# Performance work log

Measured on AMD Instinct MI355X. Metric: run time of the kernel, lower is better.

## Reference

```python
import jax, jax.numpy as jnp
import numpy as np

# ---- static config (matches init_kwargs) ----
BATCH = 8; SEQ_LEN = 1024; ENC_IN = 7; PRED_LEN = 96
D_MODEL = 512; N_HEADS = 8; D_HEAD = D_MODEL // N_HEADS
D_FF = 2048; E_LAYERS = 2; FACTOR = 5
PATCH = 16; STRIDE = 8; PAD = 8
N_PATCH = (SEQ_LEN + PAD - PATCH) // STRIDE + 1  # 128
NF = D_MODEL * N_PATCH


def _sin_pe(n, d):
    # sinusoidal positional embedding (Informer/TSLib PositionalEmbedding)
    pos = np.arange(n, dtype=np.float32)[:, None]
    div = np.exp(np.arange(0, d, 2, dtype=np.float32) * (-np.log(10000.0) / d))
    pe = np.zeros((n, d), dtype=np.float32)
    pe[:, 0::2] = np.sin(pos * div)
    pe[:, 1::2] = np.cos(pos * div)
    return jnp.asarray(pe)


def _ln(x, g, b, eps=1e-5):
    m = x.mean(-1, keepdims=True)
    v = x.var(-1, keepdims=True)
    return (x - m) / jnp.sqrt(v + eps) * g + b


def _prob_attention(q, k, v, layer_idx):
    # Informer ProbAttention, mask_flag=False. q,k,v: [B,H,L,Dh]
    B, H, L, Dh = q.shape
    u = min(int(FACTOR * np.ceil(np.log(L))), L)  # sample_k == n_top here (L_Q == L_K)
    skey = jax.random.fold_in(jax.random.key(42), layer_idx)
    samp = jax.random.randint(skey, (L, u), 0, L)          # random keys per query
    k_s = k[:, :, samp, :]                                  # [B,H,L,u,Dh]
    qk_s = jnp.einsum('bhld,bhlsd->bhls', q, k_s)           # sampled scores
    M = qk_s.max(-1) - qk_s.mean(-1)                        # sparsity measure [B,H,L]
    top = jax.lax.top_k(M, u)[1]                            # active query idx [B,H,u]
    q_r = jnp.take_along_axis(q, top[..., None], axis=2)    # [B,H,u,Dh]
    scores = jnp.einsum('bhud,bhld->bhul', q_r, k) / jnp.sqrt(jnp.asarray(Dh, q.dtype))
    attn = jax.nn.softmax(scores, axis=-1)
    upd = jnp.einsum('bhul,bhld->bhud', attn, v)            # [B,H,u,Dh]
    ctx = jnp.broadcast_to(v.mean(axis=2, keepdims=True), (B, H, L, Dh))
    bi = jnp.arange(B)[:, None, None]
    hi = jnp.arange(H)[None, :, None]
    ctx = ctx.at[bi, hi, top].set(upd)                      # scatter updated queries
    return ctx


def reference(x_enc, x_mark_enc, x_dec, x_mark_dec, patch_W,
              Wq, bq, Wk, bk, Wv, bv, Wo, bo,
              c1W, c1b, c2W, c2b, ln1g, ln1b, ln2g, ln2b,
              encg, encb, headW, headb):
    B, L, C = x_enc.shape
    # Normalize('Stat'): per-series mean/std over time
    mean = x_enc.mean(axis=1, keepdims=True)
    std = jnp.sqrt(x_enc.var(axis=1, keepdims=True) + 1e-5)
    xn = (x_enc - mean) / std
    # PatchEmbedding: [B,C,L] -> replication-pad -> unfold -> linear + pos emb
    xc = jnp.pad(xn.transpose(0, 2, 1), ((0, 0), (0, 0), (0, PAD)), mode='edge')
    idx = np.arange(N_PATCH)[:, None] * STRIDE + np.arange(PATCH)
    tok = xc[:, :, idx].reshape(B * C, N_PATCH, PATCH) @ patch_W.T  # [BC,N,dm]
    tok = tok + _sin_pe(N_PATCH, D_MODEL)
    # Transformer encoder with ProbAttention
    for l in range(E_LAYERS):
        Beff, N, _ = tok.shape
        q = (tok @ Wq[l].T + bq[l]).reshape(Beff, N, N_HEADS, D_HEAD).transpose(0, 2, 1, 3)
        k = (tok @ Wk[l].T + bk[l]).reshape(Beff, N, N_HEADS, D_HEAD).transpose(0, 2, 1, 3)
        v = (tok @ Wv[l].T + bv[l]).reshape(Beff, N, N_HEADS, D_HEAD).transpose(0, 2, 1, 3)
        ctx = _prob_attention(q, k, v, l).transpose(0, 2, 1, 3).reshape(Beff, N, D_MODEL)
        x1 = _ln(tok + ctx @ Wo[l].T + bo[l], ln1g[l], ln1b[l])
        y = jax.nn.gelu(x1 @ c1W[l].T + c1b[l], approximate=False)  # conv1d k=1 == linear
        y = y @ c2W[l].T + c2b[l]
        tok = _ln(x1 + y, ln2g[l], ln2b[l])
    tok = _ln(tok, encg, encb)
    # FlattenHead: [B,C,N,dm] -> [B,C,dm,N] -> flatten -> linear -> [B,pred,C]
    feat = tok.reshape(B, C, N_PATCH, D_MODEL).transpose(0, 1, 3, 2).reshape(B, C, NF)
    dec = (feat @ headW.T + headb).transpose(0, 2, 1)
    return dec * std + mean  # de-normalize


def setup_inputs():
    key = jax.random.key(0)
    ks = iter(jax.random.split(key, 40))
    def rn(shape, s=0.02):
        return jax.random.normal(next(ks), shape, jnp.float32) * s
    return {
        'x_enc': jax.random.normal(next(ks), (BATCH, SEQ_LEN, ENC_IN), jnp.float32),
        'x_mark_enc': jax.random.normal(next(ks), (BATCH, SEQ_LEN, 4), jnp.float32),
        'x_dec': jax.random.normal(next(ks), (BATCH, 144, ENC_IN), jnp.float32),
        'x_mark_dec': jax.random.normal(next(ks), (BATCH, 144, 4), jnp.float32),
        'patch_W': rn((D_MODEL, PATCH)),
        'Wq': rn((E_LAYERS, D_MODEL, D_MODEL)), 'bq': jnp.zeros((E_LAYERS, D_MODEL)),
        'Wk': rn((E_LAYERS, D_MODEL, D_MODEL)), 'bk': jnp.zeros((E_LAYERS, D_MODEL)),
        'Wv': rn((E_LAYERS, D_MODEL, D_MODEL)), 'bv': jnp.zeros((E_LAYERS, D_MODEL)),
        'Wo': rn((E_LAYERS, D_MODEL, D_MODEL)), 'bo': jnp.zeros((E_LAYERS, D_MODEL)),
        'c1W': rn((E_LAYERS, D_FF, D_MODEL)), 'c1b': jnp.zeros((E_LAYERS, D_FF)),
        'c2W': rn((E_LAYERS, D_MODEL, D_FF)), 'c2b': jnp.zeros((E_LAYERS, D_MODEL)),
        'ln1g': jnp.ones((E_LAYERS, D_MODEL)), 'ln1b': jnp.zeros((E_LAYERS, D_MODEL)),
        'ln2g': jnp.ones((E_LAYERS, D_MODEL)), 'ln2b': jnp.zeros((E_LAYERS, D_MODEL)),
        'encg': jnp.ones((D_MODEL,)), 'encb': jnp.zeros((D_MODEL,)),
        'headW': rn((PRED_LEN, NF)), 'headb': jnp.zeros((PRED_LEN,)),
    }
```

## Files before the change

kernel.cpp:

```cpp
#include <hip/hip_runtime.h>
#include <math.h>
#include <stdint.h>

#define SEQ   1024
#define CIN   7
#define NB    8
#define BC    56
#define NP    128
#define DM    512
#define NH    8
#define DH    64
#define DFF   2048
#define U     25
#define NTOK  (BC*NP)
#define PE_COEF (-9.210340371976184f / 512.0f)
#define HKB   256
#define HNB   256

typedef __attribute__((ext_vector_type(8))) short short8;
typedef __attribute__((ext_vector_type(4))) float f32x4;

__device__ __forceinline__ short f2bf(float x) {
    union { float f; uint32_t u; } v; v.f = x;
    uint32_t r = v.u + 0x7FFFu + ((v.u >> 16) & 1u);
    return (short)(r >> 16);
}
__device__ __forceinline__ float bf2f(short x) {
    union { uint32_t u; float f; } v; v.u = ((uint32_t)(uint16_t)x) << 16;
    return v.f;
}

__device__ __forceinline__ void gl_lds16(const void* g, void* s) {
    __builtin_amdgcn_global_load_lds((const __attribute__((address_space(1))) void*)g,
                                     (__attribute__((address_space(3))) void*)s, 16, 0, 0);
}

__global__ void stats_kernel(const float* __restrict__ x, float* __restrict__ mean,
                             float* __restrict__ stdv) {
    int bc = blockIdx.x; int b = bc / CIN, c = bc % CIN;
    const float* base = x + (size_t)b * SEQ * CIN + c;
    float s = 0.f, ss = 0.f;
    for (int i = threadIdx.x; i < SEQ; i += 256) {
        float v = base[(size_t)i * CIN];
        s += v; ss += v * v;
    }
    __shared__ float rs[256], rss[256];
    rs[threadIdx.x] = s; rss[threadIdx.x] = ss; __syncthreads();
    for (int o = 128; o > 0; o >>= 1) {
        if (threadIdx.x < o) { rs[threadIdx.x] += rs[threadIdx.x + o]; rss[threadIdx.x] += rss[threadIdx.x + o]; }
        __syncthreads();
    }
    if (threadIdx.x == 0) {
        float m = rs[0] / SEQ;
        float v = rss[0] / SEQ - m * m;
        mean[bc] = m;
        stdv[bc] = sqrtf(v + 1e-5f);
    }
}

__device__ __forceinline__ void tf_round(uint32_t& x0, uint32_t& x1, uint32_t r) {
    x0 += x1; x1 = (x1 << r) | (x1 >> (32u - r)); x1 ^= x0;
}
__device__ void threefry2x32(uint32_t k0, uint32_t k1, uint32_t x0, uint32_t x1,
                             uint32_t& o0, uint32_t& o1) {
    uint32_t ks[3] = { k0, k1, k0 ^ k1 ^ 0x1BD11BDAu };
    x0 += ks[0]; x1 += ks[1];
    const uint32_t rotA[4] = {13u, 15u, 26u, 6u}, rotB[4] = {17u, 29u, 16u, 24u};
    #pragma unroll
    for (int i = 0; i < 5; i++) {
        const uint32_t* rr = (i & 1) ? rotB : rotA;
        tf_round(x0, x1, rr[0]); tf_round(x0, x1, rr[1]);
        tf_round(x0, x1, rr[2]); tf_round(x0, x1, rr[3]);
        x0 += ks[(i + 1) % 3];
        x1 += ks[(i + 2) % 3] + (uint32_t)(i + 1);
    }
    o0 = x0; o1 = x1;
}

__global__ void prep_weights(const float* __restrict__ Wq, const float* __restrict__ Wk,
                             const float* __restrict__ Wv, const float* __restrict__ bq,
                             const float* __restrict__ bk, const float* __restrict__ bv,
                             const float* __restrict__ Wo, const float* __restrict__ c1W,
                             const float* __restrict__ c2W,
                             short* __restrict__ wqkv, float* __restrict__ bqkv,
                             short* __restrict__ wo_b, short* __restrict__ c1w_b,
                             short* __restrict__ c2w_b, int* __restrict__ samp) {
    int blk = blockIdx.x, tid = threadIdx.x;
    if (blk < 1536) {
        int idx = blk * 256 + tid;
        int k4 = idx & 127;
        int n  = (idx >> 7) % 1536;
        int l  = idx / (1536 * 128);
        int sel3 = n >> 9;
        int nn = n & 511;
        const float* src = sel3 == 0 ? Wq : sel3 == 1 ? Wk : Wv;
        float4 v = *(const float4*)(src + ((size_t)l * DM + nn) * DM + k4 * 4);
        short4 o; o.x = f2bf(v.x); o.y = f2bf(v.y); o.z = f2bf(v.z); o.w = f2bf(v.w);
        *(short4*)(wqkv + ((size_t)l * 1536 + n) * DM + k4 * 4) = o;
        if (k4 == 0) {
            const float* bsrc = sel3 == 0 ? bq : sel3 == 1 ? bk : bv;
            bqkv[l * 1536 + n] = bsrc[l * DM + nn];
        }
    } else if (blk < 6144) {
        const float* in; short* out; int i;
        if (blk < 2048)      { in = Wo;  out = wo_b;  i = (blk - 1536) * 256 + tid; }
        else if (blk < 4096) { in = c1W; out = c1w_b; i = (blk - 2048) * 256 + tid; }
        else                 { in = c2W; out = c2w_b; i = (blk - 4096) * 256 + tid; }
        float4 v = ((const float4*)in)[i];
        short4 o; o.x = f2bf(v.x); o.y = f2bf(v.y); o.z = f2bf(v.z); o.w = f2bf(v.w);
        ((short4*)out)[i] = o;
    } else {
        int l = blk - 6144;
        uint32_t s0, s1; threefry2x32(0u, 42u, 0u, (uint32_t)l, s0, s1);
        uint32_t a0, a1, b0, b1;
        threefry2x32(s0, s1, 0u, 2u, a0, a1);
        threefry2x32(s0, s1, 1u, 3u, b0, b1);
        uint32_t k20 = a1, k21 = b1;
        for (int i = tid; i < 1600; i += 256) {
            uint32_t o0, o1;
            threefry2x32(k20, k21, (uint32_t)i, (uint32_t)(1600 + i), o0, o1);
            samp[l * 3200 + i]        = (int)(o0 & 127u);
            samp[l * 3200 + 1600 + i] = (int)(o1 & 127u);
        }
    }
}

__global__ void patch_embed(const float* __restrict__ x, const float* __restrict__ pw,
                            const float* __restrict__ mean, const float* __restrict__ stdv,
                            short* __restrict__ tokb) {
    int p = blockIdx.x, bc = blockIdx.y;
    int b = bc / CIN, c = bc % CIN;
    __shared__ float xs[16];
    if (threadIdx.x < 16) {
        int i = p * 8 + threadIdx.x;
        if (i > SEQ - 1) i = SEQ - 1;
        xs[threadIdx.x] = (x[(size_t)b * SEQ * CIN + (size_t)i * CIN + c] - mean[bc]) / stdv[bc];
    }
    __syncthreads();
    for (int d = threadIdx.x; d < DM; d += blockDim.x) {
        float acc = 0.f;
        const float* wr = pw + d * 16;
        #pragma unroll
        for (int t = 0; t < 16; t++) acc += xs[t] * wr[t];
        int k2 = d & ~1;
        float ang = (float)p * __expf((float)k2 * PE_COEF);
        acc += (d & 1) ? __cosf(ang) : __sinf(ang);
        tokb[((size_t)bc * NP + p) * DM + d] = f2bf(acc);
    }
}

template<int ACT>
__global__ __launch_bounds__(256) void gemm_mfma(const short* __restrict__ A,
                                                 const short* __restrict__ W,
                                                 const float* __restrict__ bias,
                                                 short* __restrict__ Cb,
                                                 int M, int N, int K) {
    __shared__ short LDSU[2][16384];
    int tid = threadIdx.x;
    int w = tid >> 6, lane = tid & 63;
    int row0 = blockIdx.x * 128, col0 = blockIdx.y * 128;
    int wrow = (w >> 1) * 64, wcol = (w & 1) * 64;
    int nt = K >> 6;
    f32x4 acc[4][4] = {};

    auto stage = [&](int b, int kt) {
        #pragma unroll
        for (int i = 0; i < 4; i++) {
            int L = i * 4096 + w * 1024 + lane * 16;
            int row = L >> 7;
            int cb  = L & 127;
            int scb = cb ^ ((row & 7) << 4);
            gl_lds16(A + (size_t)(row0 + row) * K + kt + (scb >> 1),
                     (char*)&LDSU[b][0] + i * 4096 + w * 1024);
            gl_lds16(W + (size_t)(col0 + row) * K + kt + (scb >> 1),
                     (char*)&LDSU[b][8192] + i * 4096 + w * 1024);
        }
    };

    stage(0, 0);
    __syncthreads();
    int cur = 0;
    for (int t = 0; t < nt; t++) {
        if (t + 1 < nt) stage(cur ^ 1, (t + 1) * 64);
        const char* Ab = (const char*)&LDSU[cur][0];
        const char* Bb = (const char*)&LDSU[cur][8192];
        #pragma unroll
        for (int ks = 0; ks < 2; ks++) {
            int cb = ks * 64 + ((lane >> 4) << 4);
            short8 af[4], bfr[4];
            #pragma unroll
            for (int m = 0; m < 4; m++) {
                int r = wrow + m * 16 + (lane & 15);
                af[m] = *(const short8*)(Ab + r * 128 + (cb ^ ((r & 7) << 4)));
            }
            #pragma unroll
            for (int n = 0; n < 4; n++) {
                int r = wcol + n * 16 + (lane & 15);
                bfr[n] = *(const short8*)(Bb + r * 128 + (cb ^ ((r & 7) << 4)));
            }
            #pragma unroll
            for (int m = 0; m < 4; m++)
                #pragma unroll
                for (int n = 0; n < 4; n++)
                    acc[m][n] = __builtin_amdgcn_mfma_f32_16x16x32_bf16(af[m], bfr[n], acc[m][n], 0, 0, 0);
        }
        __syncthreads();
        cur ^= 1;
    }

    #pragma unroll
    for (int m = 0; m < 4; m++) {
        int rbase = row0 + wrow + m * 16 + ((lane >> 4) << 2);
        #pragma unroll
        for (int n = 0; n < 4; n++) {
            int col = col0 + wcol + n * 16 + (lane & 15);
            float bval = bias[col];
            #pragma unroll
            for (int j = 0; j < 4; j++) {
                float v = acc[m][n][j] + bval;
                if (ACT == 1) {
                    float u = 0.7978845608f * (v + 0.044715f * v * v * v);
                    float e = exp2f(2.8853900817779268f * u);
                    v = v - v / (e + 1.0f);
                }
                Cb[(size_t)(rbase + j) * N + col] = f2bf(v);
            }
        }
    }
}

__global__ __launch_bounds__(256) void gemm_mfma64(const short* __restrict__ A,
                                                   const short* __restrict__ W,
                                                   const float* __restrict__ bias,
                                                   const short* __restrict__ residb,
                                                   short* __restrict__ Cb,
                                                   int M, int N, int K) {
    __shared__ short LDSU[2][12288];
    int tid = threadIdx.x;
    int w = tid >> 6, lane = tid & 63;
    int row0 = blockIdx.x * 64, col0 = blockIdx.y * 128;
    int nt = K >> 6;
    f32x4 acc[4][2] = {};

    auto stage = [&](int b, int kt) {
        #pragma unroll
        for (int i = 0; i < 2; i++) {
            int L = (i * 4 + w) * 1024 + lane * 16;
            int row = L >> 7, cb = L & 127;
            int scb = cb ^ ((row & 7) << 4);
            gl_lds16(A + (size_t)(row0 + row) * K + kt + (scb >> 1),
                     (char*)&LDSU[b][0] + (i * 4 + w) * 1024);
        }
        #pragma unroll
        for (int i = 0; i < 4; i++) {
            int L = (i * 4 + w) * 1024 + lane * 16;
            int row = L >> 7, cb = L & 127;
            int scb = cb ^ ((row & 7) << 4);
            gl_lds16(W + (size_t)(col0 + row) * K + kt + (scb >> 1),
                     (char*)&LDSU[b][4096] + (i * 4 + w) * 1024);
        }
    };

    stage(0, 0);
    __syncthreads();
    int cur = 0;
    for (int t = 0; t < nt; t++) {
        if (t + 1 < nt) stage(cur ^ 1, (t + 1) * 64);
        const char* Ab = (const char*)&LDSU[cur][0];
        const char* Bb = (const char*)&LDSU[cur][4096];
        #pragma unroll
        for (int ks = 0; ks < 2; ks++) {
            int cb = ks * 64 + ((lane >> 4) << 4);
            short8 af[4], bfr[2];
            #pragma unroll
            for (int m = 0; m < 4; m++) {
                int r = m * 16 + (lane & 15);
                af[m] = *(const short8*)(Ab + r * 128 + (cb ^ ((r & 7) << 4)));
            }
            #pragma unroll
            for (int n = 0; n < 2; n++) {
                int r = w * 32 + n * 16 + (lane & 15);
                bfr[n] = *(const short8*)(Bb + r * 128 + (cb ^ ((r & 7) << 4)));
            }
            #pragma unroll
            for (int m = 0; m < 4; m++)
                #pragma unroll
                for (int n = 0; n < 2; n++)
                    acc[m][n] = __builtin_amdgcn_mfma_f32_16x16x32_bf16(af[m], bfr[n], acc[m][n], 0, 0, 0);
        }
        __syncthreads();
        cur ^= 1;
    }

    #pragma unroll
    for (int m = 0; m < 4; m++) {
        int rbase = row0 + m * 16 + ((lane >> 4) << 2);
        #pragma unroll
        for (int n = 0; n < 2; n++) {
            int col = col0 + w * 32 + n * 16 + (lane & 15);
            float bval = bias[col];
            #pragma unroll
            for (int j = 0; j < 4; j++) {
                float v = acc[m][n][j] + bval + bf2f(residb[(size_t)(rbase + j) * N + col]);
                Cb[(size_t)(rbase + j) * N + col] = f2bf(v);
            }
        }
    }
}

__global__ __launch_bounds__(256, 2) void attn_fused(const short* __restrict__ qkvb,
                                                     const int* __restrict__ samp,
                                                     short* __restrict__ ctxb) {
    __shared__ float Sbuf[64 * 130];
    __shared__ short Vt[64 * 128];
    __shared__ short Kls[128 * 64];
    __shared__ float Mv[128];
    __shared__ int   topl[32];
    __shared__ float vmean[64];
    __shared__ float vpart[256];

    float* Stop = Sbuf;
    short* Pb   = (short*)(Sbuf + 32 * 130);

    int bh = blockIdx.x, bc = bh >> 3, h = bh & 7;
    int tid = threadIdx.x, w = tid >> 6, lane = tid & 63;
    const short* base = qkvb + (size_t)bc * NP * 1536 + h * DH;
    short* cbase = ctxb + (size_t)bc * NP * DM + h * DH;

    for (int e = tid; e < 1024; e += 256) {
        int row = e >> 3, c8 = e & 7;
        short8 kv = *(const short8*)(base + (size_t)row * 1536 + 512 + c8 * 8);
        *(short8*)((char*)Kls + row * 128 + ((c8 * 16) ^ ((row & 7) << 4))) = kv;
        short8 vv = *(const short8*)(base + (size_t)row * 1536 + 1024 + c8 * 8);
        #pragma unroll
        for (int j = 0; j < 8; j++) {
            int d = c8 * 8 + j;
            *(short*)((char*)Vt + d * 256 + ((2 * row) ^ ((d & 7) << 4))) = vv[j];
        }
    }
    __syncthreads();
    {
        int d = tid & 63, part = tid >> 6;
        float s = 0.f;
        #pragma unroll
        for (int i4 = 0; i4 < 4; i4++) {
            short8 v = *(const short8*)((char*)Vt + d * 256 + ((part * 64 + i4 * 16) ^ ((d & 7) << 4)));
            #pragma unroll
            for (int j = 0; j < 8; j++) s += bf2f(v[j]);
        }
        vpart[part * 64 + d] = s;
    }

    for (int half = 0; half < 2; half++) {
        int ar = half * 64 + 16 * w + (lane & 15);
        const short* qp = base + (size_t)ar * 1536;
        short8 a0 = *(const short8*)(qp + (lane >> 4) * 8);
        short8 a1 = *(const short8*)(qp + 32 + (lane >> 4) * 8);
        #pragma unroll 2
        for (int ct = 0; ct < 8; ct++) {
            int br = ct * 16 + (lane & 15);
            int cb0 = (lane >> 4) * 16;
            short8 b0 = *(const short8*)((char*)Kls + br * 128 + (cb0 ^ ((br & 7) << 4)));
            short8 b1 = *(const short8*)((char*)Kls + br * 128 + ((cb0 + 64) ^ ((br & 7) << 4)));
            f32x4 acc = {};
            acc = __builtin_amdgcn_mfma_f32_16x16x32_bf16(a0, b0, acc, 0, 0, 0);
            acc = __builtin_amdgcn_mfma_f32_16x16x32_bf16(a1, b1, acc, 0, 0, 0);
            int r0 = 16 * w + ((lane >> 4) << 2);
            int c = ct * 16 + (lane & 15);
            #pragma unroll
            for (int j = 0; j < 4; j++) Sbuf[(r0 + j) * 130 + c] = acc[j] * 0.125f;
        }
        __syncthreads();
        if (tid < 64) {
            int r = half * 64 + tid;
            const int* sp = samp + r * U;
            const float* Srow = &Sbuf[tid * 130];
            float mx = -1e30f, sm = 0.f;
            #pragma unroll
            for (int s = 0; s < U; s++) { float v = Srow[sp[s]]; mx = fmaxf(mx, v); sm += v; }
            Mv[r] = mx - sm * (1.0f / U);
        } else if (half == 0 && tid < 128) {
            int d = tid - 64;
            vmean[d] = (vpart[d] + vpart[64 + d] + vpart[128 + d] + vpart[192 + d]) * (1.0f / 128.0f);
        }
        __syncthreads();
    }

    if (w == 0) {
        float v0 = Mv[lane], v1 = Mv[lane + 64];
        for (int it = 0; it < U; it++) {
            float bv; int bi;
            if (v1 > v0) { bv = v1; bi = lane + 64; } else { bv = v0; bi = lane; }
            #pragma unroll
            for (int o = 32; o > 0; o >>= 1) {
                float ov = __shfl_xor(bv, o);
                int   oi = __shfl_xor(bi, o);
                if (ov > bv || (ov == bv && oi < bi)) { bv = ov; bi = oi; }
            }
            if (lane == 0) topl[it] = bi;
            if (bi == lane) v0 = -1e30f;
            if (bi == lane + 64) v1 = -1e30f;
        }
    } else {
        for (int e = tid - 64; e < 128 * 16; e += 192) {
            int n = e >> 4, c4 = e & 15;
            short4 o;
            o.x = f2bf(vmean[c4 * 4 + 0]); o.y = f2bf(vmean[c4 * 4 + 1]);
            o.z = f2bf(vmean[c4 * 4 + 2]); o.w = f2bf(vmean[c4 * 4 + 3]);
            *(short4*)(cbase + (size_t)n * DM + c4 * 4) = o;
        }
    }
    __syncthreads();

    {
        int rt = w & 1, cth = w >> 1;
        int u = rt * 16 + (lane & 15);
        int qrow = topl[u < U ? u : U - 1];
        const short* qp = base + (size_t)qrow * 1536;
        short8 a0 = *(const short8*)(qp + (lane >> 4) * 8);
        short8 a1 = *(const short8*)(qp + 32 + (lane >> 4) * 8);
        #pragma unroll
        for (int cti = 0; cti < 4; cti++) {
            int ct = cth * 4 + cti;
            int br = ct * 16 + (lane & 15);
            int cb0 = (lane >> 4) * 16;
            short8 b0 = *(const short8*)((char*)Kls + br * 128 + (cb0 ^ ((br & 7) << 4)));
            short8 b1 = *(const short8*)((char*)Kls + br * 128 + ((cb0 + 64) ^ ((br & 7) << 4)));
            f32x4 acc = {};
            acc = __builtin_amdgcn_mfma_f32_16x16x32_bf16(a0, b0, acc, 0, 0, 0);
            acc = __builtin_amdgcn_mfma_f32_16x16x32_bf16(a1, b1, acc, 0, 0, 0);
            int r0 = rt * 16 + ((lane >> 4) << 2);
            int c = ct * 16 + (lane & 15);
            #pragma unroll
            for (int j = 0; j < 4; j++) Stop[(r0 + j) * 130 + c] = acc[j] * 0.125f;
        }
    }
    __syncthreads();

    for (int e = tid; e < 7 * 128; e += 256)
        Pb[(25 + (e >> 7)) * 128 + (e & 127)] = 0;
    for (int it = w; it < U; it += 4) {
        float s0 = Stop[it * 130 + lane], s1 = Stop[it * 130 + 64 + lane];
        float mx = fmaxf(s0, s1);
        #pragma unroll
        for (int o = 32; o > 0; o >>= 1) mx = fmaxf(mx, __shfl_xor(mx, o));
        float e0 = expf(s0 - mx), e1 = expf(s1 - mx);
        float sum = e0 + e1;
        #pragma unroll
        for (int o = 32; o > 0; o >>= 1) sum += __shfl_xor(sum, o);
        float inv = 1.0f / sum;
        int sw = (it & 7) << 4;
        *(short*)((char*)Pb + it * 256 + ((2 * lane) ^ sw))        = f2bf(e0 * inv);
        *(short*)((char*)Pb + it * 256 + ((2 * (64 + lane)) ^ sw)) = f2bf(e1 * inv);
    }
    __syncthreads();

    #pragma unroll
    for (int t = w * 2; t < w * 2 + 2; t++) {
        int rt = t >> 2, ct = t & 3;
        int pr = rt * 16 + (lane & 15);
        int vr = ct * 16 + (lane & 15);
        f32x4 acc = {};
        #pragma unroll
        for (int ks = 0; ks < 4; ks++) {
            int off = ks * 64 + (lane >> 4) * 16;
            short8 a = *(const short8*)((char*)Pb + pr * 256 + (off ^ ((pr & 7) << 4)));
            short8 b = *(const short8*)((char*)Vt + vr * 256 + (off ^ ((vr & 7) << 4)));
            acc = __builtin_amdgcn_mfma_f32_16x16x32_bf16(a, b, acc, 0, 0, 0);
        }
        int u0 = rt * 16 + ((lane >> 4) << 2), d = ct * 16 + (lane & 15);
        #pragma unroll
        for (int j = 0; j < 4; j++) {
            int u = u0 + j;
            if (u < U) cbase[(size_t)topl[u] * DM + d] = f2bf(acc[j]);
        }
    }
}

__global__ __launch_bounds__(256) void residual_ln(const short* __restrict__ a,
                                                   const float* __restrict__ g,
                                                   const float* __restrict__ beta,
                                                   short* __restrict__ outb) {
    int row = blockIdx.x;
    int tid = threadIdx.x;
    uint32_t va = ((const uint32_t*)(a + (size_t)row * DM))[tid];
    float x0 = bf2f((short)(va & 0xffff));
    float x1 = bf2f((short)(va >> 16));
    __shared__ float rs[256], rss[256];
    rs[tid] = x0 + x1; rss[tid] = x0 * x0 + x1 * x1; __syncthreads();
    for (int o = 128; o > 0; o >>= 1) {
        if (tid < o) { rs[tid] += rs[tid + o]; rss[tid] += rss[tid + o]; }
        __syncthreads();
    }
    float m = rs[0] / DM;
    float var = rss[0] / DM - m * m;
    float r = rsqrtf(var + 1e-5f);
    float2 gg = ((const float2*)g)[tid];
    float2 bb = ((const float2*)beta)[tid];
    float y0 = (x0 - m) * r * gg.x + bb.x;
    float y1 = (x1 - m) * r * gg.y + bb.y;
    uint32_t vo = (uint32_t)(uint16_t)f2bf(y0) | ((uint32_t)(uint16_t)f2bf(y1) << 16);
    ((uint32_t*)(outb + (size_t)row * DM))[tid] = vo;
}

__global__ void transpose_tok(const short* __restrict__ tokb, short* __restrict__ featb) {
    __shared__ short t[32][34];
    int bc = blockIdx.z, dt = blockIdx.y, pt = blockIdx.x;
    int tx = threadIdx.x, ty = threadIdx.y;
    #pragma unroll
    for (int i = 0; i < 4; i++) {
        int p = pt * 32 + ty + i * 8;
        int d = dt * 32 + tx;
        t[ty + i * 8][tx] = tokb[((size_t)bc * NP + p) * DM + d];
    }
    __syncthreads();
    #pragma unroll
    for (int i = 0; i < 4; i++) {
        int d = dt * 32 + ty + i * 8;
        int p = pt * 32 + tx;
        featb[(size_t)bc * (DM * NP) + (size_t)d * NP + p] = t[tx][ty + i * 8];
    }
}

__global__ __launch_bounds__(256) void head_mfma(const float* __restrict__ hw,
                                                 const short* __restrict__ featb,
                                                 float* __restrict__ partial) {
    __shared__ short Als[96 * 64];
    __shared__ short Bls[64 * 64];
    int tid = threadIdx.x;
    int w = tid >> 6, lane = tid & 63;
    int wm = w >> 1, wn = w & 1;
    int kb = blockIdx.x * HKB;
    f32x4 acc[3][2] = {};
    const char* Ab = (const char*)Als;
    const char* Bb = (const char*)Bls;

    for (int kt = 0; kt < HKB; kt += 64) {
        #pragma unroll
        for (int i = 0; i < 6; i++) {
            int s = tid + i * 256;
            int row = s >> 4, c4 = s & 15;
            float4 v = *(const float4*)(hw + (size_t)row * 65536 + kb + kt + c4 * 4);
            short4 o; o.x = f2bf(v.x); o.y = f2bf(v.y); o.z = f2bf(v.z); o.w = f2bf(v.w);
            int boff = row * 128 + ((c4 * 8) ^ ((row & 7) << 4));
            *(short4*)((char*)Als + boff) = o;
        }
        #pragma unroll
        for (int i = 0; i < 4; i++) {
            int s = tid + i * 256;
            int row = s >> 4, c4 = s & 15;
            short4 o;
            if (row < BC) o = *(const short4*)(featb + (size_t)row * 65536 + kb + kt + c4 * 4);
            else { o.x = 0; o.y = 0; o.z = 0; o.w = 0; }
            int boff = row * 128 + ((c4 * 8) ^ ((row & 7) << 4));
            *(short4*)((char*)Bls + boff) = o;
        }
        __syncthreads();
        #pragma unroll
        for (int ks = 0; ks < 2; ks++) {
            int cb = ks * 64 + ((lane >> 4) << 4);
            short8 af[3], bfr[2];
            #pragma unroll
            for (int m = 0; m < 3; m++) {
                int r = wm * 48 + m * 16 + (lane & 15);
                af[m] = *(const short8*)(Ab + r * 128 + (cb ^ ((r & 7) << 4)));
            }
            #pragma unroll
            for (int n = 0; n < 2; n++) {
                int r = wn * 32 + n * 16 + (lane & 15);
                bfr[n] = *(const short8*)(Bb + r * 128 + (cb ^ ((r & 7) << 4)));
            }
            #pragma unroll
            for (int m = 0; m < 3; m++)
                #pragma unroll
                for (int n = 0; n < 2; n++)
                    acc[m][n] = __builtin_amdgcn_mfma_f32_16x16x32_bf16(af[m], bfr[n], acc[m][n], 0, 0, 0);
        }
        __syncthreads();
    }

    float* pb = partial + (size_t)blockIdx.x * (96 * 64);
    #pragma unroll
    for (int m = 0; m < 3; m++) {
        int rbase = wm * 48 + m * 16 + ((lane >> 4) << 2);
        #pragma unroll
        for (int n = 0; n < 2; n++) {
            int col = wn * 32 + n * 16 + (lane & 15);
            #pragma unroll
            for (int j = 0; j < 4; j++)
                pb[(rbase + j) * 64 + col] = acc[m][n][j];
        }
    }
}

__global__ void finalize_a(const float* __restrict__ partial, float* __restrict__ p2) {
    int i = blockIdx.x * 256 + threadIdx.x;
    int s = blockIdx.y;
    const float* p = partial + (size_t)s * 32 * 6144 + i;
    float sum = 0.f;
    #pragma unroll
    for (int b = 0; b < 32; b++) sum += p[(size_t)b * 6144];
    p2[s * 6144 + i] = sum;
}

__global__ void finalize_b(const float* __restrict__ p2, const float* __restrict__ hb,
                           const float* __restrict__ mean, const float* __restrict__ stdv,
                           float* __restrict__ out) {
    int i = blockIdx.x * 256 + threadIdx.x;
    if (i >= NB * 96 * CIN) return;
    int b = i / (96 * CIN);
    int r = i % (96 * CIN);
    int t = r / CIN, c = r % CIN;
    int bc = b * CIN + c;
    int j = t * 64 + bc;
    float s = 0.f;
    #pragma unroll
    for (int k = 0; k < 8; k++) s += p2[k * 6144 + j];
    out[i] = (s + hb[t]) * stdv[bc] + mean[bc];
}

extern "C" void kernel_launch(void* const* d_in, const int* in_sizes, int n_in,
                              void* d_out, int out_size, void* d_ws, size_t ws_size,
                              hipStream_t stream) {
    (void)in_sizes; (void)n_in; (void)out_size; (void)ws_size;
    const float* x_enc   = (const float*)d_in[0];
    const float* patch_W = (const float*)d_in[4];
    const float* Wq  = (const float*)d_in[5];
    const float* bq  = (const float*)d_in[6];
    const float* Wk  = (const float*)d_in[7];
    const float* bk  = (const float*)d_in[8];
    const float* Wv  = (const float*)d_in[9];
    const float* bv  = (const float*)d_in[10];
    const float* Wo  = (const float*)d_in[11];
    const float* bo  = (const float*)d_in[12];
    const float* c1W = (const float*)d_in[13];
    const float* c1b = (const float*)d_in[14];
    const float* c2W = (const float*)d_in[15];
    const float* c2b = (const float*)d_in[16];
    const float* ln1g = (const float*)d_in[17];
    const float* ln1b = (const float*)d_in[18];
    const float* ln2g = (const float*)d_in[19];
    const float* ln2b = (const float*)d_in[20];
    const float* encg = (const float*)d_in[21];
    const float* encb = (const float*)d_in[22];
    const float* headW = (const float*)d_in[23];
    const float* headb = (const float*)d_in[24];
    float* out = (float*)d_out;

    float* ws = (float*)d_ws;
    float* mean = ws + 0;
    float* stdv = ws + 64;
    float* bqkv = ws + 128;
    int*   samp = (int*)(ws + 6144);
    size_t off = 32768;
    const size_t T = (size_t)NTOK * DM;
    float* partial = ws + off; off += T;
    float* p2      = ws + off; off += 65536;
    short* sbase = (short*)(ws + off);
    size_t soff = 0;
    short* tok_b  = sbase + soff; soff += T;
    short* ctx_b  = sbase + soff; soff += T;
    short* x1_b   = sbase + soff; soff += T;
    short* pA_b   = sbase + soff; soff += T;
    short* qkv_b  = sbase + soff; soff += 3 * T;
    short* ffn_b  = sbase + soff; soff += (size_t)NTOK * DFF;
    short* featb  = ffn_b;
    short* wqkv_b = sbase + soff; soff += 2 * 1536 * DM;
    short* wo_b   = sbase + soff; soff += 2 * DM * DM;
    short* c1w_b  = sbase + soff; soff += 2 * (size_t)DFF * DM;
    short* c2w_b  = sbase + soff; soff += 2 * (size_t)DM * DFF;

    stats_kernel<<<BC, 256, 0, stream>>>(x_enc, mean, stdv);
    prep_weights<<<6146, 256, 0, stream>>>(Wq, Wk, Wv, bq, bk, bv, Wo, c1W, c2W,
                                           wqkv_b, bqkv, wo_b, c1w_b, c2w_b, samp);
    patch_embed<<<dim3(NP, BC), 128, 0, stream>>>(x_enc, patch_W, mean, stdv, tok_b);

    for (int l = 0; l < 2; l++) {
        gemm_mfma<0><<<dim3(56, 12), 256, 0, stream>>>(tok_b, wqkv_b + (size_t)l * 1536 * DM, bqkv + l * 1536, qkv_b, NTOK, 1536, DM);
        attn_fused<<<448, 256, 0, stream>>>(qkv_b, samp + l * 3200, ctx_b);
        gemm_mfma64<<<dim3(112, 4), 256, 0, stream>>>(ctx_b, wo_b + (size_t)l * DM * DM, bo + l * DM, tok_b, pA_b, NTOK, DM, DM);
        residual_ln<<<NTOK, 256, 0, stream>>>(pA_b, ln1g + l * DM, ln1b + l * DM, x1_b);
        gemm_mfma<1><<<dim3(56, 16), 256, 0, stream>>>(x1_b, c1w_b + (size_t)l * DFF * DM, c1b + l * DFF, ffn_b, NTOK, DFF, DM);
        gemm_mfma64<<<dim3(112, 4), 256, 0, stream>>>(ffn_b, c2w_b + (size_t)l * DM * DFF, c2b + l * DM, x1_b, pA_b, NTOK, DM, DFF);
        residual_ln<<<NTOK, 256, 0, stream>>>(pA_b, ln2g + l * DM, ln2b + l * DM, tok_b);
    }

    residual_ln<<<NTOK, 256, 0, stream>>>(tok_b, encg, encb, x1_b);
    transpose_tok<<<dim3(4, 16, BC), dim3(32, 8), 0, stream>>>(x1_b, featb);
    head_mfma<<<HNB, 256, 0, stream>>>(headW, featb, partial);
    finalize_a<<<dim3(24, 8), 256, 0, stream>>>(partial, p2);
    finalize_b<<<21, 256, 0, stream>>>(p2, headb, mean, stdv, out);
}
```

Measured before the change: 309.3 us.

## Fuse stats into prep, warp-level LayerNorm, fuse final LN with transpose, single finalize

```diff
diff --git a/kernel.cpp b/kernel.cpp
--- a/kernel.cpp
+++ b/kernel.cpp
@@ -35,29 +35,6 @@
                                      (__attribute__((address_space(3))) void*)s, 16, 0, 0);
 }
 
-__global__ void stats_kernel(const float* __restrict__ x, float* __restrict__ mean,
-                             float* __restrict__ stdv) {
-    int bc = blockIdx.x; int b = bc / CIN, c = bc % CIN;
-    const float* base = x + (size_t)b * SEQ * CIN + c;
-    float s = 0.f, ss = 0.f;
-    for (int i = threadIdx.x; i < SEQ; i += 256) {
-        float v = base[(size_t)i * CIN];
-        s += v; ss += v * v;
-    }
-    __shared__ float rs[256], rss[256];
-    rs[threadIdx.x] = s; rss[threadIdx.x] = ss; __syncthreads();
-    for (int o = 128; o > 0; o >>= 1) {
-        if (threadIdx.x < o) { rs[threadIdx.x] += rs[threadIdx.x + o]; rss[threadIdx.x] += rss[threadIdx.x + o]; }
-        __syncthreads();
-    }
-    if (threadIdx.x == 0) {
-        float m = rs[0] / SEQ;
-        float v = rss[0] / SEQ - m * m;
-        mean[bc] = m;
-        stdv[bc] = sqrtf(v + 1e-5f);
-    }
-}
-
 __device__ __forceinline__ void tf_round(uint32_t& x0, uint32_t& x1, uint32_t r) {
     x0 += x1; x1 = (x1 << r) | (x1 >> (32u - r)); x1 ^= x0;
 }
@@ -81,10 +58,11 @@
                              const float* __restrict__ Wv, const float* __restrict__ bq,
                              const float* __restrict__ bk, const float* __restrict__ bv,
                              const float* __restrict__ Wo, const float* __restrict__ c1W,
-                             const float* __restrict__ c2W,
+                             const float* __restrict__ c2W, const float* __restrict__ x_enc,
                              short* __restrict__ wqkv, float* __restrict__ bqkv,
                              short* __restrict__ wo_b, short* __restrict__ c1w_b,
-                             short* __restrict__ c2w_b, int* __restrict__ samp) {
+                             short* __restrict__ c2w_b, int* __restrict__ samp,
+                             float* __restrict__ mean, float* __restrict__ stdv) {
     int blk = blockIdx.x, tid = threadIdx.x;
     if (blk < 1536) {
         int idx = blk * 256 + tid;
@@ -109,7 +87,7 @@
         float4 v = ((const float4*)in)[i];
         short4 o; o.x = f2bf(v.x); o.y = f2bf(v.y); o.z = f2bf(v.z); o.w = f2bf(v.w);
         ((short4*)out)[i] = o;
-    } else {
+    } else if (blk < 6146) {
         int l = blk - 6144;
         uint32_t s0, s1; threefry2x32(0u, 42u, 0u, (uint32_t)l, s0, s1);
         uint32_t a0, a1, b0, b1;
@@ -121,6 +99,27 @@
             threefry2x32(k20, k21, (uint32_t)i, (uint32_t)(1600 + i), o0, o1);
             samp[l * 3200 + i]        = (int)(o0 & 127u);
             samp[l * 3200 + 1600 + i] = (int)(o1 & 127u);
+        }
+    } else {
+        int bc = blk - 6146;
+        int b = bc / CIN, c = bc % CIN;
+        const float* base = x_enc + (size_t)b * SEQ * CIN + c;
+        float s = 0.f, ss = 0.f;
+        for (int i = tid; i < SEQ; i += 256) {
+            float v = base[(size_t)i * CIN];
+            s += v; ss += v * v;
+        }
+        __shared__ float rs[256], rss[256];
+        rs[tid] = s; rss[tid] = ss; __syncthreads();
+        for (int o = 128; o > 0; o >>= 1) {
+            if (tid < o) { rs[tid] += rs[tid + o]; rss[tid] += rss[tid + o]; }
+            __syncthreads();
+        }
+        if (tid == 0) {
+            float m = rs[0] / SEQ;
+            float v = rss[0] / SEQ - m * m;
+            mean[bc] = m;
+            stdv[bc] = sqrtf(v + 1e-5f);
         }
     }
 }
@@ -477,48 +476,83 @@
     }
 }
 
-__global__ __launch_bounds__(256) void residual_ln(const short* __restrict__ a,
-                                                   const float* __restrict__ g,
-                                                   const float* __restrict__ beta,
-                                                   short* __restrict__ outb) {
-    int row = blockIdx.x;
-    int tid = threadIdx.x;
-    uint32_t va = ((const uint32_t*)(a + (size_t)row * DM))[tid];
-    float x0 = bf2f((short)(va & 0xffff));
-    float x1 = bf2f((short)(va >> 16));
-    __shared__ float rs[256], rss[256];
-    rs[tid] = x0 + x1; rss[tid] = x0 * x0 + x1 * x1; __syncthreads();
-    for (int o = 128; o > 0; o >>= 1) {
-        if (tid < o) { rs[tid] += rs[tid + o]; rss[tid] += rss[tid + o]; }
-        __syncthreads();
-    }
-    float m = rs[0] / DM;
-    float var = rss[0] / DM - m * m;
+__global__ __launch_bounds__(256) void ln4(const short* __restrict__ a,
+                                           const float* __restrict__ g,
+                                           const float* __restrict__ beta,
+                                           short* __restrict__ outb) {
+    int w = threadIdx.x >> 6, lane = threadIdx.x & 63;
+    size_t row = (size_t)blockIdx.x * 4 + w;
+    short8 v = *(const short8*)(a + row * DM + lane * 8);
+    float x[8];
+    float s = 0.f, ss = 0.f;
+    #pragma unroll
+    for (int j = 0; j < 8; j++) { x[j] = bf2f(v[j]); s += x[j]; ss += x[j] * x[j]; }
+    #pragma unroll
+    for (int o = 32; o > 0; o >>= 1) { s += __shfl_xor(s, o); ss += __shfl_xor(ss, o); }
+    float m = s * (1.0f / DM);
+    float var = ss * (1.0f / DM) - m * m;
     float r = rsqrtf(var + 1e-5f);
-    float2 gg = ((const float2*)g)[tid];
-    float2 bb = ((const float2*)beta)[tid];
-    float y0 = (x0 - m) * r * gg.x + bb.x;
-    float y1 = (x1 - m) * r * gg.y + bb.y;
-    uint32_t vo = (uint32_t)(uint16_t)f2bf(y0) | ((uint32_t)(uint16_t)f2bf(y1) << 16);
-    ((uint32_t*)(outb + (size_t)row * DM))[tid] = vo;
-}
-
-__global__ void transpose_tok(const short* __restrict__ tokb, short* __restrict__ featb) {
-    __shared__ short t[32][34];
-    int bc = blockIdx.z, dt = blockIdx.y, pt = blockIdx.x;
-    int tx = threadIdx.x, ty = threadIdx.y;
-    #pragma unroll
-    for (int i = 0; i < 4; i++) {
-        int p = pt * 32 + ty + i * 8;
-        int d = dt * 32 + tx;
-        t[ty + i * 8][tx] = tokb[((size_t)bc * NP + p) * DM + d];
+    float4 g0 = *(const float4*)(g + lane * 8);
+    float4 g1 = *(const float4*)(g + lane * 8 + 4);
+    float4 b0 = *(const float4*)(beta + lane * 8);
+    float4 b1 = *(const float4*)(beta + lane * 8 + 4);
+    float gv[8] = {g0.x, g0.y, g0.z, g0.w, g1.x, g1.y, g1.z, g1.w};
+    float bv[8] = {b0.x, b0.y, b0.z, b0.w, b1.x, b1.y, b1.z, b1.w};
+    short8 o8;
+    #pragma unroll
+    for (int j = 0; j < 8; j++) o8[j] = f2bf((x[j] - m) * r * gv[j] + bv[j]);
+    *(short8*)(outb + row * DM + lane * 8) = o8;
+}
+
+__global__ __launch_bounds__(256) void ln_transpose(const short* __restrict__ tokb,
+                                                    const float* __restrict__ g,
+                                                    const float* __restrict__ beta,
+                                                    short* __restrict__ featb) {
+    __shared__ short t[32][520];
+    int pt = blockIdx.x, bc = blockIdx.y;
+    int w = threadIdx.x >> 6, lane = threadIdx.x & 63;
+    float4 g0 = *(const float4*)(g + lane * 8);
+    float4 g1 = *(const float4*)(g + lane * 8 + 4);
+    float4 be0 = *(const float4*)(beta + lane * 8);
+    float4 be1 = *(const float4*)(beta + lane * 8 + 4);
+    float gv[8] = {g0.x, g0.y, g0.z, g0.w, g1.x, g1.y, g1.z, g1.w};
+    float bv[8] = {be0.x, be0.y, be0.z, be0.w, be1.x, be1.y, be1.z, be1.w};
+    #pragma unroll
+    for (int i = 0; i < 8; i++) {
+        int pr = w * 8 + i;
+        size_t row = (size_t)bc * NP + pt * 32 + pr;
+        short8 v = *(const short8*)(tokb + row * DM + lane * 8);
+        float x[8];
+        float s = 0.f, ss = 0.f;
+        #pragma unroll
+        for (int j = 0; j < 8; j++) { x[j] = bf2f(v[j]); s += x[j]; ss += x[j] * x[j]; }
+        #pragma unroll
+        for (int o = 32; o > 0; o >>= 1) { s += __shfl_xor(s, o); ss += __shfl_xor(ss, o); }
+        float m = s * (1.0f / DM);
+        float var = ss * (1.0f / DM) - m * m;
+        float r = rsqrtf(var + 1e-5f);
+        short8 o8;
+        #pragma unroll
+        for (int j = 0; j < 8; j++) o8[j] = f2bf((x[j] - m) * r * gv[j] + bv[j]);
+        *(short8*)(&t[pr][lane * 8]) = o8;
     }
     __syncthreads();
     #pragma unroll
-    for (int i = 0; i < 4; i++) {
-        int d = dt * 32 + ty + i * 8;
-        int p = pt * 32 + tx;
-        featb[(size_t)bc * (DM * NP) + (size_t)d * NP + p] = t[tx][ty + i * 8];
+    for (int dd = 0; dd < 2; dd++) {
+        int d = threadIdx.x * 2 + dd;
+        uint32_t pk[16];
+        #pragma unroll
+        for (int p2 = 0; p2 < 16; p2++) {
+            uint32_t lo = (uint16_t)t[2 * p2][d];
+            uint32_t hi = (uint16_t)t[2 * p2 + 1][d];
+            pk[p2] = lo | (hi << 16);
+        }
+        uint32_t* dst = (uint32_t*)(featb + (size_t)bc * (DM * NP) + (size_t)d * NP + pt * 32);
+        #pragma unroll
+        for (int q = 0; q < 4; q++) {
+            int4 val; val.x = pk[q*4]; val.y = pk[q*4+1]; val.z = pk[q*4+2]; val.w = pk[q*4+3];
+            *(int4*)(dst + q * 4) = val;
+        }
     }
 }
 
@@ -593,19 +627,9 @@
     }
 }
 
-__global__ void finalize_a(const float* __restrict__ partial, float* __restrict__ p2) {
-    int i = blockIdx.x * 256 + threadIdx.x;
-    int s = blockIdx.y;
-    const float* p = partial + (size_t)s * 32 * 6144 + i;
-    float sum = 0.f;
-    #pragma unroll
-    for (int b = 0; b < 32; b++) sum += p[(size_t)b * 6144];
-    p2[s * 6144 + i] = sum;
-}
-
-__global__ void finalize_b(const float* __restrict__ p2, const float* __restrict__ hb,
-                           const float* __restrict__ mean, const float* __restrict__ stdv,
-                           float* __restrict__ out) {
+__global__ void finalize(const float* __restrict__ partial, const float* __restrict__ hb,
+                         const float* __restrict__ mean, const float* __restrict__ stdv,
+                         float* __restrict__ out) {
     int i = blockIdx.x * 256 + threadIdx.x;
     if (i >= NB * 96 * CIN) return;
     int b = i / (96 * CIN);
@@ -614,8 +638,7 @@
     int bc = b * CIN + c;
     int j = t * 64 + bc;
     float s = 0.f;
-    #pragma unroll
-    for (int k = 0; k < 8; k++) s += p2[k * 6144 + j];
+    for (int blk = 0; blk < HNB; blk++) s += partial[(size_t)blk * 6144 + j];
     out[i] = (s + hb[t]) * stdv[bc] + mean[bc];
 }
 
@@ -655,7 +678,6 @@
     size_t off = 32768;
     const size_t T = (size_t)NTOK * DM;
     float* partial = ws + off; off += T;
-    float* p2      = ws + off; off += 65536;
     short* sbase = (short*)(ws + off);
     size_t soff = 0;
     short* tok_b  = sbase + soff; soff += T;
@@ -670,24 +692,21 @@
     short* c1w_b  = sbase + soff; soff += 2 * (size_t)DFF * DM;
     short* c2w_b  = sbase + soff; soff += 2 * (size_t)DM * DFF;
 
-    stats_kernel<<<BC, 256, 0, stream>>>(x_enc, mean, stdv);
-    prep_weights<<<6146, 256, 0, stream>>>(Wq, Wk, Wv, bq, bk, bv, Wo, c1W, c2W,
-                                           wqkv_b, bqkv, wo_b, c1w_b, c2w_b, samp);
+    prep_weights<<<6202, 256, 0, stream>>>(Wq, Wk, Wv, bq, bk, bv, Wo, c1W, c2W, x_enc,
+                                           wqkv_b, bqkv, wo_b, c1w_b, c2w_b, samp, mean, stdv);
     patch_embed<<<dim3(NP, BC), 128, 0, stream>>>(x_enc, patch_W, mean, stdv, tok_b);
 
     for (int l = 0; l < 2; l++) {
         gemm_mfma<0><<<dim3(56, 12), 256, 0, stream>>>(tok_b, wqkv_b + (size_t)l * 1536 * DM, bqkv + l * 1536, qkv_b, NTOK, 1536, DM);
         attn_fused<<<448, 256, 0, stream>>>(qkv_b, samp + l * 3200, ctx_b);
         gemm_mfma64<<<dim3(112, 4), 256, 0, stream>>>(ctx_b, wo_b + (size_t)l * DM * DM, bo + l * DM, tok_b, pA_b, NTOK, DM, DM);
-        residual_ln<<<NTOK, 256, 0, stream>>>(pA_b, ln1g + l * DM, ln1b + l * DM, x1_b);
+        ln4<<<NTOK / 4, 256, 0, stream>>>(pA_b, ln1g + l * DM, ln1b + l * DM, x1_b);
         gemm_mfma<1><<<dim3(56, 16), 256, 0, stream>>>(x1_b, c1w_b + (size_t)l * DFF * DM, c1b + l * DFF, ffn_b, NTOK, DFF, DM);
         gemm_mfma64<<<dim3(112, 4), 256, 0, stream>>>(ffn_b, c2w_b + (size_t)l * DM * DFF, c2b + l * DM, x1_b, pA_b, NTOK, DM, DFF);
-        residual_ln<<<NTOK, 256, 0, stream>>>(pA_b, ln2g + l * DM, ln2b + l * DM, tok_b);
-    }
-
-    residual_ln<<<NTOK, 256, 0, stream>>>(tok_b, encg, encb, x1_b);
-    transpose_tok<<<dim3(4, 16, BC), dim3(32, 8), 0, stream>>>(x1_b, featb);
+        ln4<<<NTOK / 4, 256, 0, stream>>>(pA_b, ln2g + l * DM, ln2b + l * DM, tok_b);
+    }
+
+    ln_transpose<<<dim3(4, BC), 256, 0, stream>>>(tok_b, encg, encb, featb);
     head_mfma<<<HNB, 256, 0, stream>>>(headW, featb, partial);
-    finalize_a<<<dim3(24, 8), 256, 0, stream>>>(partial, p2);
-    finalize_b<<<21, 256, 0, stream>>>(p2, headb, mean, stdv, out);
-}
+    finalize<<<21, 256, 0, stream>>>(partial, headb, mean, stdv, out);
+}
```

Result: faster. 300.6 us (-2.8%).
